# Kernel tuning notes

Measured on AMD Instinct MI355X. Metric: run time of the kernel, lower is better.

Reference implementation:

```python
import jax, jax.numpy as jnp
import numpy as np

EPS = 1e-5
NH = 8          # num_heads
WT_LEVELS = 5


def ln(x, w, b):
    m = jnp.mean(x, -1, keepdims=True)
    v = jnp.mean((x - m) ** 2, -1, keepdims=True)
    return (x - m) / jnp.sqrt(v + EPS) * w + b


def gelu(x):
    return jax.nn.gelu(x, approximate=False)  # torch nn.GELU default (erf)


def dwconv(x, w, b, stride, padding):
    # x: [B,C,H,W], w: [kh,kw,1,C] depthwise
    C = x.shape[1]
    y = jax.lax.conv_general_dilated(x, w, (stride, stride), padding,
                                     dimension_numbers=('NCHW', 'HWIO', 'NCHW'),
                                     feature_group_count=C)
    return y if b is None else y + b[None, :, None, None]


def conv2d(x, w, b, padding='SAME'):
    y = jax.lax.conv_general_dilated(x, w, (1, 1), padding,
                                     dimension_numbers=('NCHW', 'HWIO', 'NCHW'))
    return y + b[None, :, None, None]


def haar_dwt(x):
    # orthonormal 2x2 Haar analysis via even/odd slicing (no conv needed)
    a = x[..., 0::2, 0::2]; b = x[..., 0::2, 1::2]
    c = x[..., 1::2, 0::2]; d = x[..., 1::2, 1::2]
    ll = (a + b + c + d) * 0.5
    lh = (-a - b + c + d) * 0.5
    hl = (-a + b - c + d) * 0.5
    hh = (a - b - c + d) * 0.5
    return ll, lh, hl, hh


def haar_idwt(ll, lh, hl, hh):
    a = (ll - lh - hl + hh) * 0.5
    b = (ll - lh + hl - hh) * 0.5
    c = (ll + lh - hl - hh) * 0.5
    d = (ll + lh + hl + hh) * 0.5
    B, C, H, W = ll.shape
    top = jnp.stack([a, b], -1).reshape(B, C, H, 2 * W)
    bot = jnp.stack([c, d], -1).reshape(B, C, H, 2 * W)
    return jnp.stack([top, bot], -2).reshape(B, C, 2 * H, 2 * W)


def wtconv(x, base_w, base_b, base_scale, wav_w, wav_scale):
    # WTConv2d (Haar, wt_levels=5, kernel 3, depthwise): multi-level wavelet
    # decomposition, depthwise 3x3 conv + scale at each level, reconstruction,
    # added to a scaled depthwise base conv.
    B, C = x.shape[0], x.shape[1]
    lls, hs, shapes = [], [], []
    cur = x
    for i in range(WT_LEVELS):
        shapes.append(cur.shape)
        Hc, Wc = cur.shape[2], cur.shape[3]
        if Hc % 2 or Wc % 2:
            cur = jnp.pad(cur, ((0, 0), (0, 0), (0, Hc % 2), (0, Wc % 2)))
        sub = jnp.stack(haar_dwt(cur), 2)                # [B,C,4,h,w]
        cur = sub[:, :, 0]
        h, w = sub.shape[3], sub.shape[4]
        t = sub.reshape(B, C * 4, h, w)
        t = dwconv(t, wav_w[i], None, 1, 'SAME') * wav_scale[i][None, :, None, None]
        t = t.reshape(B, C, 4, h, w)
        lls.append(t[:, :, 0])
        hs.append(t[:, :, 1:4])
    nxt = 0.0
    for i in range(WT_LEVELS - 1, -1, -1):
        ll = lls[i] + nxt
        h3 = hs[i]
        nxt = haar_idwt(ll, h3[:, :, 0], h3[:, :, 1], h3[:, :, 2])
        sh = shapes[i]
        nxt = nxt[:, :, :sh[2], :sh[3]]
    base = dwconv(x, base_w, base_b, 1, 'SAME') * base_scale[None, :, None, None]
    return base + nxt


def block_forward(x, H, W, ln1_w, ln1_b, ln2_w, ln2_b, q_w, kv1_w, kv2_w,
                  sr1_w, sr1_b, sr2_w, sr2_b, an1_w, an1_b, an2_w, an2_b,
                  wt_base_w, wt_base_b, wt_base_scale, wt_wav_w, wt_wav_scale,
                  cp2d_w, cp2d_b, cn_w, cn_b, proj_w, proj_b,
                  fc1_w, fc1_b, fc2_w, fc2_b):
    B, N, C0 = x.shape
    Cp = C0 // 4            # conv/wavelet part channels
    Ca = C0 - Cp            # attention part channels (3/4)
    hd = Ca // NH
    scale = hd ** -0.5

    xin = ln(x, ln1_w, ln1_b)
    xc, xa = xin[..., :Cp], xin[..., Cp:]

    # --- wavelet-conv branch ---
    xc = xc.reshape(B, H, W, Cp).transpose(0, 3, 1, 2)        # [B,Cp,H,W]
    xc = wtconv(xc, wt_base_w, wt_base_b, wt_base_scale, wt_wav_w, wt_wav_scale)
    xc = conv2d(xc, cp2d_w, cp2d_b, 'SAME')                   # k3 p1 (sr_ratio=8)
    xc = gelu(ln(xc.reshape(B, Cp, N).transpose(0, 2, 1), cn_w, cn_b))  # [B,N,Cp]

    # --- multi-scale spatial-reduction attention (sr_ratio=8) ---
    q = (xa @ q_w).reshape(B, N, NH, hd).transpose(0, 2, 1, 3)  # [B,NH,N,hd]
    x_ = xa.transpose(0, 2, 1).reshape(B, Ca, H, W)
    x1 = gelu(ln(dwconv(x_, sr1_w, sr1_b, 8, 'VALID').reshape(B, Ca, -1)
                 .transpose(0, 2, 1), an1_w, an1_b))           # [B,49,Ca]
    x2 = gelu(ln(dwconv(x_, sr2_w, sr2_b, 4, 'VALID').reshape(B, Ca, -1)
                 .transpose(0, 2, 1), an2_w, an2_b))           # [B,196,Ca]

    def branch(xs, kv_w, qh):
        L = xs.shape[1]
        kv = (xs @ kv_w).reshape(B, L, 2, NH // 2, hd).transpose(2, 0, 3, 1, 4)
        k, v = kv[0], kv[1]
        a = jax.nn.softmax(jnp.einsum('bhnd,bhld->bhnl', qh, k) * scale, axis=-1)
        return jnp.einsum('bhnl,bhld->bhnd', a, v).transpose(0, 2, 1, 3).reshape(B, N, Ca // 2)

    y1 = branch(x1, kv1_w, q[:, :NH // 2])
    y2 = branch(x2, kv2_w, q[:, NH // 2:])

    attn_out = jnp.concatenate([y1, y2, xc], -1) @ proj_w + proj_b

    x = x + attn_out
    m = ln(x, ln2_w, ln2_b)
    return x + (gelu(m @ fc1_w + fc1_b) @ fc2_w + fc2_b)


def setup_inputs() -> dict:
    key = jax.random.key(0)
    ks = jax.random.split(key, 16)
    B, H, W, C0 = 32, 56, 56, 128
    N = H * W
    Cp, Ca = C0 // 4, C0 // 4 * 3

    def nrm(k, shape, std=0.02):
        return jax.random.normal(k, shape, jnp.float32) * std

    return dict(
        x=jax.random.normal(ks[0], (B, N, C0), jnp.float32),
        H=H, W=W,
        ln1_w=jnp.ones((C0,)), ln1_b=jnp.zeros((C0,)),
        ln2_w=jnp.ones((C0,)), ln2_b=jnp.zeros((C0,)),
        q_w=nrm(ks[1], (Ca, Ca)),
        kv1_w=nrm(ks[2], (Ca, Ca)),
        kv2_w=nrm(ks[3], (Ca, Ca)),
        sr1_w=nrm(ks[4], (8, 8, 1, Ca), 0.05), sr1_b=jnp.zeros((Ca,)),
        sr2_w=nrm(ks[5], (4, 4, 1, Ca), 0.05), sr2_b=jnp.zeros((Ca,)),
        an1_w=jnp.ones((Ca,)), an1_b=jnp.zeros((Ca,)),
        an2_w=jnp.ones((Ca,)), an2_b=jnp.zeros((Ca,)),
        wt_base_w=nrm(ks[6], (3, 3, 1, Cp), 0.1), wt_base_b=jnp.zeros((Cp,)),
        wt_base_scale=jnp.ones((Cp,)),
        wt_wav_w=nrm(ks[7], (5, 3, 3, 1, 4 * Cp), 0.1),
        wt_wav_scale=jnp.full((5, 4 * Cp), 0.1, jnp.float32),
        cp2d_w=nrm(ks[8], (3, 3, Cp, Cp), 0.05), cp2d_b=jnp.zeros((Cp,)),
        cn_w=jnp.ones((Cp,)), cn_b=jnp.zeros((Cp,)),
        proj_w=nrm(ks[9], (C0, C0)), proj_b=jnp.zeros((C0,)),
        fc1_w=nrm(ks[10], (C0, 4 * C0)), fc1_b=jnp.zeros((4 * C0,)),
        fc2_w=nrm(ks[11], (4 * C0, C0)), fc2_b=jnp.zeros((C0,)),
    )


def reference(x, H, W, ln1_w, ln1_b, ln2_w, ln2_b, q_w, kv1_w, kv2_w,
              sr1_w, sr1_b, sr2_w, sr2_b, an1_w, an1_b, an2_w, an2_b,
              wt_base_w, wt_base_b, wt_base_scale, wt_wav_w, wt_wav_scale,
              cp2d_w, cp2d_b, cn_w, cn_b, proj_w, proj_b,
              fc1_w, fc1_b, fc2_w, fc2_b):
    return block_forward(x, H, W, ln1_w, ln1_b, ln2_w, ln2_b, q_w, kv1_w, kv2_w,
                         sr1_w, sr1_b, sr2_w, sr2_b, an1_w, an1_b, an2_w, an2_b,
                         wt_base_w, wt_base_b, wt_base_scale, wt_wav_w, wt_wav_scale,
                         cp2d_w, cp2d_b, cn_w, cn_b, proj_w, proj_b,
                         fc1_w, fc1_b, fc2_w, fc2_b)
```

## Files before the change

kernel.cpp:

```cpp
#include <hip/hip_runtime.h>
#include <hip/hip_bf16.h>
#include <math.h>

typedef __hip_bfloat16 bf16;
typedef __attribute__((ext_vector_type(8))) short bf16x8;
typedef __attribute__((ext_vector_type(4))) float f32x4;

#define Bc   32
#define Hc   56
#define Wcc  56
#define Nc   3136
#define Cpc  32
#define Cac  96
#define EPSc 1e-5f
#define SCALEc 0.28867513459481287f

__device__ __forceinline__ float gelu_f(float x) {
    return 0.5f * x * (1.0f + erff(x * 0.7071067811865475f));
}

__device__ __forceinline__ float fast_exp2(float x) {
#if defined(__has_builtin)
#if __has_builtin(__builtin_amdgcn_exp2f)
    return __builtin_amdgcn_exp2f(x);
#else
    return exp2f(x);
#endif
#else
    return exp2f(x);
#endif
}

__global__ __launch_bounds__(256) void ln1_kernel(const float* __restrict__ x,
        const float* __restrict__ g, const float* __restrict__ be,
        float* __restrict__ xa, bf16* __restrict__ xab, float* __restrict__ xc_img)
{
    int wv = threadIdx.x >> 6, lane = threadIdx.x & 63;
    int row = blockIdx.x * 4 + wv;
    if (row >= Bc * Nc) return;
    const float* xr = x + (size_t)row * 128;
    float x0 = xr[lane];
    float x1 = xr[lane + 64];
    float s = x0 + x1, q = x0 * x0 + x1 * x1;
    for (int o = 32; o; o >>= 1) { s += __shfl_xor(s, o); q += __shfl_xor(q, o); }
    float mean = s * (1.f / 128.f);
    float inv = rsqrtf(q * (1.f / 128.f) - mean * mean + EPSc);
    int b = row / Nc, n = row % Nc;
    {
        int c = lane;
        float y = (x0 - mean) * inv * g[c] + be[c];
        if (c < Cpc) xc_img[(size_t)(b * Cpc + c) * Nc + n] = y;
        else { xa[(size_t)row * Cac + (c - Cpc)] = y;
               xab[(size_t)row * Cac + (c - Cpc)] = __float2bfloat16(y); }
    }
    {
        int c = lane + 64;
        float y = (x1 - mean) * inv * g[c] + be[c];
        xa[(size_t)row * Cac + (c - Cpc)] = y;
        xab[(size_t)row * Cac + (c - Cpc)] = __float2bfloat16(y);
    }
}

__global__ void dwt_kernel(const float* __restrict__ src, int cs, int h, int w,
                           int h2, int w2, float* __restrict__ sub)
{
    int t = blockIdx.x * blockDim.x + threadIdx.x;
    int total = Bc * 32 * h2 * w2;
    if (t >= total) return;
    int xx = t % w2; int r = t / w2;
    int yy = r % h2; r /= h2;
    int c = r & 31; int b = r >> 5;
    const float* sp = src + (size_t)cs * (b * 32 + c) * h * w;
    int y0 = yy * 2, x0 = xx * 2;
    bool xe = (x0 + 1 < w), ye = (y0 + 1 < h);
    float a  = sp[y0 * w + x0];
    float bb = xe ? sp[y0 * w + x0 + 1] : 0.f;
    float cc = ye ? sp[(y0 + 1) * w + x0] : 0.f;
    float dd = (xe && ye) ? sp[(y0 + 1) * w + x0 + 1] : 0.f;
    size_t pl = (size_t)h2 * w2;
    size_t ob = (size_t)(b * 128 + c * 4) * pl + yy * w2 + xx;
    sub[ob]          = ( a + bb + cc + dd) * 0.5f;
    sub[ob + pl]     = (-a - bb + cc + dd) * 0.5f;
    sub[ob + 2 * pl] = (-a + bb - cc + dd) * 0.5f;
    sub[ob + 3 * pl] = ( a - bb - cc + dd) * 0.5f;
}

template<int H>
__device__ __forceinline__ void dw3_body(int r, const float* __restrict__ src,
        const float* __restrict__ wt, const float* __restrict__ scale,
        float* __restrict__ dst)
{
    int x = r % H; int rr = r / H;
    int y = rr % H; rr /= H;
    int c = rr & 127;
    const float* sp = src + (r - x - y * H);
    float acc = 0.f;
    #pragma unroll
    for (int u = 0; u < 3; u++) {
        int yy = y + u - 1;
        if (yy < 0 || yy >= H) continue;
        #pragma unroll
        for (int v = 0; v < 3; v++) {
            int xx = x + v - 1;
            if (xx < 0 || xx >= H) continue;
            acc += sp[yy * H + xx] * wt[(u * 3 + v) * 128 + c];
        }
    }
    dst[r] = acc * scale[c];
}

__global__ void dw3x3_all_kernel(const float* __restrict__ sub, const float* __restrict__ wavw,
        const float* __restrict__ wavs, float* __restrict__ tt)
{
    int t = blockIdx.x * blockDim.x + threadIdx.x;
    if (t < 3211264)      dw3_body<28>(t,           sub,           wavw,        wavs,       tt);
    else if (t < 4014080) dw3_body<14>(t - 3211264, sub + 3211264, wavw + 1152, wavs + 128, tt + 3211264);
    else if (t < 4214784) dw3_body<7> (t - 4014080, sub + 4014080, wavw + 2304, wavs + 256, tt + 4014080);
    else if (t < 4280320) dw3_body<4> (t - 4214784, sub + 4214784, wavw + 3456, wavs + 384, tt + 4214784);
    else if (t < 4296704) dw3_body<2> (t - 4280320, sub + 4280320, wavw + 4608, wavs + 512, tt + 4280320);
}

__global__ void idwt_kernel(const float* __restrict__ tl, const float* __restrict__ nxt,
        float* __restrict__ outp, int h2, int w2, int ho, int wo)
{
    int t = blockIdx.x * blockDim.x + threadIdx.x;
    int total = Bc * 32 * ho * wo;
    if (t >= total) return;
    int x = t % wo; int r = t / wo;
    int y = r % ho; r /= ho;
    int c = r & 31; int b = r >> 5;
    int y2 = y >> 1, x2 = x >> 1;
    size_t pl = (size_t)h2 * w2;
    size_t base = (size_t)(b * 128 + c * 4) * pl + y2 * w2 + x2;
    float ll = tl[base];
    if (nxt) ll += nxt[(size_t)(b * 32 + c) * pl + y2 * w2 + x2];
    float lh = tl[base + pl], hl = tl[base + 2 * pl], hh = tl[base + 3 * pl];
    float v;
    if ((y & 1) == 0) v = ((x & 1) == 0) ? (ll - lh - hl + hh) : (ll - lh + hl - hh);
    else              v = ((x & 1) == 0) ? (ll + lh - hl - hh) : (ll + lh + hl + hh);
    outp[t] = v * 0.5f;
}

__global__ void idwt_dwbase_kernel(const float* __restrict__ tl, const float* __restrict__ nxt,
        const float* __restrict__ src, const float* __restrict__ wt,
        const float* __restrict__ scale, const float* __restrict__ bias,
        bf16* __restrict__ dst_nhwc)
{
    int t = blockIdx.x * blockDim.x + threadIdx.x;
    if (t >= Bc * 32 * Nc) return;
    int x = t % Wcc; int r = t / Wcc;
    int y = r % Hc; r /= Hc;
    int c = r & 31; int b = r >> 5;
    int y2 = y >> 1, x2 = x >> 1;
    const size_t pl = 784;
    size_t base = (size_t)(b * 128 + c * 4) * pl + y2 * 28 + x2;
    float ll = tl[base] + nxt[(size_t)(b * 32 + c) * pl + y2 * 28 + x2];
    float lh = tl[base + pl], hl = tl[base + 2 * pl], hh = tl[base + 3 * pl];
    float v;
    if ((y & 1) == 0) v = ((x & 1) == 0) ? (ll - lh - hl + hh) : (ll - lh + hl - hh);
    else              v = ((x & 1) == 0) ? (ll + lh - hl - hh) : (ll + lh + hl + hh);
    float recon = v * 0.5f;
    const float* sp = src + (t - x - y * Wcc);
    float acc = 0.f;
    #pragma unroll
    for (int u = 0; u < 3; u++) {
        int yy = y + u - 1;
        if (yy < 0 || yy >= Hc) continue;
        #pragma unroll
        for (int vv2 = 0; vv2 < 3; vv2++) {
            int xx = x + vv2 - 1;
            if (xx < 0 || xx >= Wcc) continue;
            acc += sp[yy * Wcc + xx] * wt[(u * 3 + vv2) * 32 + c];
        }
    }
    acc = (acc + bias[c]) * scale[c] + recon;
    dst_nhwc[(((size_t)b * Hc + y) * Wcc + x) * 32 + c] = __float2bfloat16(acc);
}

__global__ void wprep_kernel(const float* __restrict__ qw, const float* __restrict__ kv1w,
        const float* __restrict__ kv2w, const float* __restrict__ pw,
        const float* __restrict__ f1w, const float* __restrict__ f2w,
        const float* __restrict__ cpw, bf16* __restrict__ qwt, bf16* __restrict__ kv1wt,
        bf16* __restrict__ kv2wt, bf16* __restrict__ pwt, bf16* __restrict__ w1t,
        bf16* __restrict__ w2t, bf16* __restrict__ cpwt)
{
    int t = blockIdx.x * blockDim.x + threadIdx.x;
    if (t < 9216) {
        int n = t % 96, k = t / 96;
        qwt[n * 96 + k] = __float2bfloat16(qw[t]);
    } else if (t < 18432) {
        int u = t - 9216; int n = u % 96, k = u / 96;
        kv1wt[n * 96 + k] = __float2bfloat16(kv1w[u]);
    } else if (t < 27648) {
        int u = t - 18432; int n = u % 96, k = u / 96;
        kv2wt[n * 96 + k] = __float2bfloat16(kv2w[u]);
    } else if (t < 44032) {
        int u = t - 27648; int n = u % 128, k = u / 128;
        pwt[n * 128 + k] = __float2bfloat16(pw[u]);
    } else if (t < 109568) {
        int u = t - 44032; int n = u % 512, k = u / 512;
        w1t[(size_t)n * 128 + k] = __float2bfloat16(f1w[u]);
    } else if (t < 175104) {
        int u = t - 109568; int n = u % 128, k = u / 128;
        w2t[(size_t)n * 512 + k] = __float2bfloat16(f2w[u]);
    } else if (t < 184320) {
        int u = t - 175104; int co = u / 288, k = u % 288;
        cpwt[u] = __float2bfloat16(cpw[k * 32 + co]);
    }
}

__global__ __launch_bounds__(256) void cp2d_cn_kernel(const bf16* __restrict__ src,
        const bf16* __restrict__ wtc, const float* __restrict__ bias,
        const float* __restrict__ cnw, const float* __restrict__ cnb,
        bf16* __restrict__ attn_cat)
{
    __shared__ unsigned short in_s[10 * 400];
    __shared__ unsigned short w_s[32 * 296];
    int tid = threadIdx.x;
    int b = blockIdx.y;
    int ty = blockIdx.x / 7, tx = blockIdx.x % 7;
    for (int idx = tid; idx < 1152; idx += 256) {
        int co = idx / 36, j8 = (idx % 36) * 8;
        *(int4*)&w_s[co * 296 + j8] = *(const int4*)(wtc + co * 288 + j8);
    }
    {
        int idx = tid;
        if (idx < 200) {
            int cell = idx >> 1, half = idx & 1;
            int dy = cell / 10, dx = cell % 10;
            int gy = ty * 8 - 1 + dy, gx = tx * 8 - 1 + dx;
            int4 v0 = make_int4(0, 0, 0, 0), v1 = v0;
            if (gy >= 0 && gy < 56 && gx >= 0 && gx < 56) {
                const int4* gp = (const int4*)(src + ((((size_t)b * 56 + gy) * 56 + gx) * 32 + half * 16));
                v0 = gp[0]; v1 = gp[1];
            }
            *(int4*)&in_s[dy * 400 + dx * 40 + half * 16] = v0;
            *(int4*)&in_s[dy * 400 + dx * 40 + half * 16 + 8] = v1;
        }
    }
    __syncthreads();
    int wave = tid >> 6, lane = tid & 63;
    int ml = lane & 15, qd = lane >> 4;
    int m = wave * 16 + ml;
    int ly = m >> 3, lx = m & 7;
    f32x4 acc0 = {0.f, 0.f, 0.f, 0.f}, acc1 = {0.f, 0.f, 0.f, 0.f};
    #pragma unroll
    for (int u = 0; u < 3; u++)
    #pragma unroll
    for (int v = 0; v < 3; v++) {
        bf16x8 af = *(const bf16x8*)&in_s[(ly + u) * 400 + (lx + v) * 40 + qd * 8];
        int k = (u * 3 + v) * 32 + qd * 8;
        bf16x8 b0 = *(const bf16x8*)&w_s[ml * 296 + k];
        bf16x8 b1 = *(const bf16x8*)&w_s[(16 + ml) * 296 + k];
        acc0 = __builtin_amdgcn_mfma_f32_16x16x32_bf16(af, b0, acc0, 0, 0, 0);
        acc1 = __builtin_amdgcn_mfma_f32_16x16x32_bf16(af, b1, acc1, 0, 0, 0);
    }
    float bia0 = bias[ml], bia1 = bias[16 + ml];
    float g0 = cnw[ml], g1 = cnw[16 + ml];
    float be0 = cnb[ml], be1 = cnb[16 + ml];
    #pragma unroll
    for (int r = 0; r < 4; r++) {
        float c0 = acc0[r] + bia0;
        float c1 = acc1[r] + bia1;
        float s = c0 + c1, q = c0 * c0 + c1 * c1;
        #pragma unroll
        for (int o = 8; o; o >>= 1) { s += __shfl_xor(s, o); q += __shfl_xor(q, o); }
        float mean = s * (1.f / 32.f);
        float inv = rsqrtf(q * (1.f / 32.f) - mean * mean + EPSc);
        int mr = wave * 16 + qd * 4 + r;
        int ry = ty * 8 + (mr >> 3), rx = tx * 8 + (mr & 7);
        bf16* op = attn_cat + ((size_t)b * Nc + ry * 56 + rx) * 128 + 96;
        op[ml]      = __float2bfloat16(gelu_f((c0 - mean) * inv * g0 + be0));
        op[16 + ml] = __float2bfloat16(gelu_f((c1 - mean) * inv * g1 + be1));
    }
}

template<int KS, int LD>
__device__ __forceinline__ void sr_body(int t, const float* __restrict__ xa,
        const float* __restrict__ wt, const float* __restrict__ bias,
        float* __restrict__ outp)
{
    int c = t % Cac; int r = t / Cac;
    int j = r % LD; r /= LD;
    int i = r % LD; int b = r / LD;
    float acc = bias[c];
    for (int u = 0; u < KS; u++)
        for (int v = 0; v < KS; v++)
            acc += xa[(size_t)(b * Nc + (i * KS + u) * Wcc + (j * KS + v)) * Cac + c]
                 * wt[(u * KS + v) * Cac + c];
    outp[t] = acc;
}

__global__ void sr_all_kernel(const float* __restrict__ xa,
        const float* __restrict__ sr1w, const float* __restrict__ sr1b, float* __restrict__ x1p,
        const float* __restrict__ sr2w, const float* __restrict__ sr2b, float* __restrict__ x2p)
{
    int t = blockIdx.x * blockDim.x + threadIdx.x;
    if (t < 150528) sr_body<8, 7>(t, xa, sr1w, sr1b, x1p);
    else {
        int u = t - 150528;
        if (u < 602112) sr_body<4, 14>(u, xa, sr2w, sr2b, x2p);
    }
}

__global__ __launch_bounds__(256) void ln96_all_kernel(
        const float* __restrict__ s1, const float* __restrict__ g1,
        const float* __restrict__ b1, bf16* __restrict__ d1,
        const float* __restrict__ s2, const float* __restrict__ g2,
        const float* __restrict__ b2, bf16* __restrict__ d2)
{
    int wv = threadIdx.x >> 6, lane = threadIdx.x & 63;
    int row = blockIdx.x * 4 + wv;
    const float* sp; const float* g; const float* be; bf16* dst; int r;
    if (row < 1568)      { sp = s1; g = g1; be = b1; dst = d1; r = row; }
    else if (row < 7840) { sp = s2; g = g2; be = b2; dst = d2; r = row - 1568; }
    else return;
    sp += (size_t)r * 96;
    float x0 = sp[lane];
    float x1 = (lane < 32) ? sp[64 + lane] : 0.f;
    float s = x0 + x1, q = x0 * x0 + x1 * x1;
    for (int o = 32; o; o >>= 1) { s += __shfl_xor(s, o); q += __shfl_xor(q, o); }
    float mean = s * (1.f / 96.f);
    float inv = rsqrtf(q * (1.f / 96.f) - mean * mean + EPSc);
    dst[(size_t)r * 96 + lane] =
        __float2bfloat16(gelu_f((x0 - mean) * inv * g[lane] + be[lane]));
    if (lane < 32)
        dst[(size_t)r * 96 + 64 + lane] =
            __float2bfloat16(gelu_f((x1 - mean) * inv * g[64 + lane] + be[64 + lane]));
}

__global__ __launch_bounds__(256) void ln2_kernel(const float* __restrict__ xres,
        const float* __restrict__ g, const float* __restrict__ be,
        bf16* __restrict__ xnb)
{
    int wv = threadIdx.x >> 6, lane = threadIdx.x & 63;
    int row = blockIdx.x * 4 + wv;
    if (row >= Bc * Nc) return;
    const float* xr = xres + (size_t)row * 128;
    float x0 = xr[lane], x1 = xr[lane + 64];
    float s = x0 + x1, q = x0 * x0 + x1 * x1;
    for (int o = 32; o; o >>= 1) { s += __shfl_xor(s, o); q += __shfl_xor(q, o); }
    float mean = s * (1.f / 128.f);
    float inv = rsqrtf(q * (1.f / 128.f) - mean * mean + EPSc);
    xnb[(size_t)row * 128 + lane] =
        __float2bfloat16((x0 - mean) * inv * g[lane] + be[lane]);
    xnb[(size_t)row * 128 + lane + 64] =
        __float2bfloat16((x1 - mean) * inv * g[lane + 64] + be[lane + 64]);
}

template<int NF, bool GELU, bool RES, int OMODE>
__global__ __launch_bounds__(256) void gemm_kernel(const bf16* __restrict__ A,
        const bf16* __restrict__ Wt, const float* __restrict__ bias,
        const float* __restrict__ res, void* __restrict__ outp,
        int M, int K, int Nt)
{
    constexpr int TN = 16 * NF;
    __shared__ unsigned short As[64][40];
    __shared__ unsigned short Bs[TN][40];
    int tid = threadIdx.x;
    int wave = tid >> 6, lane = tid & 63;
    int m0 = blockIdx.y * 64, n0 = blockIdx.x * TN;
    f32x4 acc[NF];
    #pragma unroll
    for (int f = 0; f < NF; f++) acc[f] = (f32x4){0.f, 0.f, 0.f, 0.f};

    int ar = tid >> 2, ac = (tid & 3) << 3;
    int ml = wave * 16 + (lane & 15);
    int qd = lane >> 4;

    for (int k0 = 0; k0 < K; k0 += 32) {
        int4 av = make_int4(0, 0, 0, 0);
        if (m0 + ar < M) av = *(const int4*)(A + (size_t)(m0 + ar) * K + k0 + ac);
        *(int4*)&As[ar][ac] = av;
        for (int idx = tid; idx < TN * 4; idx += 256) {
            int br = idx >> 2, bc = (idx & 3) << 3;
            *(int4*)&Bs[br][bc] = *(const int4*)(Wt + (size_t)(n0 + br) * K + k0 + bc);
        }
        __syncthreads();
        bf16x8 af = *(const bf16x8*)&As[ml][qd * 8];
        #pragma unroll
        for (int f = 0; f < NF; f++) {
            bf16x8 bfv = *(const bf16x8*)&Bs[f * 16 + (lane & 15)][qd * 8];
            acc[f] = __builtin_amdgcn_mfma_f32_16x16x32_bf16(af, bfv, acc[f], 0, 0, 0);
        }
        __syncthreads();
    }
    #pragma unroll
    for (int f = 0; f < NF; f++) {
        int n = n0 + f * 16 + (lane & 15);
        #pragma unroll
        for (int r = 0; r < 4; r++) {
            int m = m0 + wave * 16 + qd * 4 + r;
            if (m >= M) continue;
            float v = acc[f][r];
            if (bias) v += bias[n];
            if (GELU) v = gelu_f(v);
            if (RES)  v += res[(size_t)m * Nt + n];
            if (OMODE == 1)
                ((bf16*)outp)[(size_t)m * Nt + n] = __float2bfloat16(v);
            else if (OMODE == 2) {
                int b = m / Nc, nn = m - b * Nc;
                int h = n / 12, d = n - h * 12;
                ((float*)outp)[(((size_t)(b * 8 + h)) * Nc + nn) * 12 + d] = v;
            } else
                ((float*)outp)[(size_t)m * Nt + n] = v;
        }
    }
}

template<int L>
__device__ __forceinline__ void attn_body(const float* __restrict__ qh,
        const float* __restrict__ kv, int hl, int h, int b,
        float* kb, float* vb, bf16* __restrict__ attn_cat)
{
    for (int idx = threadIdx.x; idx < L * 3; idx += 256) {
        int l = idx / 3, f = idx % 3;
        const float4* kp = (const float4*)(kv + (size_t)(b * L + l) * 96 + hl * 12) + f;
        float4 kk = kp[0];
        float4 vv = kp[12];
        *(float4*)&kb[l * 12 + f * 4] = kk;
        *(float4*)&vb[l * 12 + f * 4] = vv;
    }
    int n = blockIdx.x * 256 + threadIdx.x;
    bool act = (n < Nc);
    int nn = act ? n : (Nc - 1);
    const float4* qp = (const float4*)(qh + (((size_t)(b * 8 + h)) * Nc + nn) * 12);
    float4 q0 = qp[0], q1 = qp[1], q2 = qp[2];
    const float PRE = SCALEc * 1.4426950408889634f;
    q0.x *= PRE; q0.y *= PRE; q0.z *= PRE; q0.w *= PRE;
    q1.x *= PRE; q1.y *= PRE; q1.z *= PRE; q1.w *= PRE;
    q2.x *= PRE; q2.y *= PRE; q2.z *= PRE; q2.w *= PRE;
    __syncthreads();

    float den = 0.f;
    float o[12];
    #pragma unroll
    for (int d = 0; d < 12; d++) o[d] = 0.f;

    #pragma unroll 4
    for (int l = 0; l < L; l++) {
        const float4 k0 = *(const float4*)&kb[l * 12];
        const float4 k1 = *(const float4*)&kb[l * 12 + 4];
        const float4 k2 = *(const float4*)&kb[l * 12 + 8];
        float s0 = q0.x * k0.x + q0.y * k0.y + q0.z * k0.z + q0.w * k0.w;
        float s1 = q1.x * k1.x + q1.y * k1.y + q1.z * k1.z + q1.w * k1.w;
        float s2 = q2.x * k2.x + q2.y * k2.y + q2.z * k2.z + q2.w * k2.w;
        float e = fast_exp2(s0 + s1 + s2);
        den += e;
        const float4 v0 = *(const float4*)&vb[l * 12];
        const float4 v1 = *(const float4*)&vb[l * 12 + 4];
        const float4 v2 = *(const float4*)&vb[l * 12 + 8];
        o[0] += e * v0.x; o[1]  += e * v0.y; o[2]  += e * v0.z; o[3]  += e * v0.w;
        o[4] += e * v1.x; o[5]  += e * v1.y; o[6]  += e * v1.z; o[7]  += e * v1.w;
        o[8] += e * v2.x; o[9]  += e * v2.y; o[10] += e * v2.z; o[11] += e * v2.w;
    }
    if (act) {
        float rden = 1.f / den;
        bf16* op = attn_cat + (size_t)(b * Nc + n) * 128 + h * 12;
        #pragma unroll
        for (int d = 0; d < 12; d++) op[d] = __float2bfloat16(o[d] * rden);
    }
}

__global__ __launch_bounds__(256) void attn_kernel(const float* __restrict__ qh,
        const float* __restrict__ kv1, const float* __restrict__ kv2,
        bf16* __restrict__ attn_cat)
{
    __shared__ float kb[196 * 12];
    __shared__ float vb[196 * 12];
    int h = blockIdx.y, b = blockIdx.z;
    if (h < 4) attn_body<49> (qh, kv1, h,     h, b, kb, vb, attn_cat);
    else       attn_body<196>(qh, kv2, h - 4, h, b, kb, vb, attn_cat);
}

extern "C" void kernel_launch(void* const* d_in, const int* in_sizes, int n_in,
                              void* d_out, int out_size, void* d_ws, size_t ws_size,
                              hipStream_t stream)
{
    const float* x    = (const float*)d_in[0];
    const float* ln1w = (const float*)d_in[3];
    const float* ln1b = (const float*)d_in[4];
    const float* ln2w = (const float*)d_in[5];
    const float* ln2b = (const float*)d_in[6];
    const float* qw   = (const float*)d_in[7];
    const float* kv1w = (const float*)d_in[8];
    const float* kv2w = (const float*)d_in[9];
    const float* sr1w = (const float*)d_in[10];
    const float* sr1b = (const float*)d_in[11];
    const float* sr2w = (const float*)d_in[12];
    const float* sr2b = (const float*)d_in[13];
    const float* an1w = (const float*)d_in[14];
    const float* an1b = (const float*)d_in[15];
    const float* an2w = (const float*)d_in[16];
    const float* an2b = (const float*)d_in[17];
    const float* wbw  = (const float*)d_in[18];
    const float* wbb  = (const float*)d_in[19];
    const float* wbs  = (const float*)d_in[20];
    const float* wavw = (const float*)d_in[21];
    const float* wavs = (const float*)d_in[22];
    const float* cpw  = (const float*)d_in[23];
    const float* cpb  = (const float*)d_in[24];
    const float* cnw  = (const float*)d_in[25];
    const float* cnb  = (const float*)d_in[26];
    const float* pw   = (const float*)d_in[27];
    const float* pb   = (const float*)d_in[28];
    const float* f1w  = (const float*)d_in[29];
    const float* f1b  = (const float*)d_in[30];
    const float* f2w  = (const float*)d_in[31];
    const float* f2b  = (const float*)d_in[32];
    float* dout = (float*)d_out;
    float* ws = (float*)d_ws;

    float* XA    = ws;
    float* QB    = ws + 9633792;
    float* XRES  = ws;
    bf16*  XNb   = (bf16*)(ws + 12845056);
    bf16*  XAb   = (bf16*)(ws + 19267584);
    bf16*  ACATb = (bf16*)(ws + 24084480);
    float* XCI   = ws + 30507008;
    float* SUB   = ws + 33718272;
    float* TT    = ws + 38014976;
    float* RA    = ws + 42311680;
    float* RB    = ws + 45522944;
    float* X1P   = ws + 48734208;
    float* X2P   = ws + 48884736;
    bf16*  X1Bb  = (bf16*)(ws + 49486848);
    bf16*  X2Bb  = (bf16*)(ws + 49562112);
    float* KV1   = ws + 49863168;
    float* KV2   = ws + 50013696;
    bf16*  WTB   = (bf16*)(ws + 50615808);
    bf16*  qwt   = WTB;
    bf16*  kv1wt = WTB + 9216;
    bf16*  kv2wt = WTB + 18432;
    bf16*  pwt   = WTB + 27648;
    bf16*  w1t   = WTB + 44032;
    bf16*  w2t   = WTB + 109568;
    bf16*  cpwt  = WTB + 175104;
    bf16*  Hb    = (bf16*)(ws + 24084480);
    bf16*  CIMGb = (bf16*)SUB;
    float* S0 = SUB;            float* T0 = TT;
    float* S1 = SUB + 3211264;  float* T1 = TT + 3211264;
    float* S2 = SUB + 4014080;  float* T2 = TT + 4014080;
    float* S3 = SUB + 4214784;  float* T3 = TT + 4214784;
    float* S4 = SUB + 4280320;  float* T4 = TT + 4280320;

    wprep_kernel<<<720, 256, 0, stream>>>(qw, kv1w, kv2w, pw, f1w, f2w, cpw,
                                          qwt, kv1wt, kv2wt, pwt, w1t, w2t, cpwt);

    ln1_kernel<<<25088, 256, 0, stream>>>(x, ln1w, ln1b, XA, XAb, XCI);

    dwt_kernel<<<3136, 256, 0, stream>>>(XCI, 1, 56, 56, 28, 28, S0);
    dwt_kernel<<<784,  256, 0, stream>>>(S0, 4, 28, 28, 14, 14, S1);
    dwt_kernel<<<196,  256, 0, stream>>>(S1, 4, 14, 14, 7, 7,   S2);
    dwt_kernel<<<64,   256, 0, stream>>>(S2, 4, 7, 7,   4, 4,   S3);
    dwt_kernel<<<16,   256, 0, stream>>>(S3, 4, 4, 4,   2, 2,   S4);

    dw3x3_all_kernel<<<16784, 256, 0, stream>>>(SUB, wavw, wavs, TT);

    idwt_kernel<<<64,   256, 0, stream>>>(T4, nullptr, RA, 2, 2, 4, 4);
    idwt_kernel<<<196,  256, 0, stream>>>(T3, RA, RB, 4, 4, 7, 7);
    idwt_kernel<<<784,  256, 0, stream>>>(T2, RB, RA, 7, 7, 14, 14);
    idwt_kernel<<<3136, 256, 0, stream>>>(T1, RA, RB, 14, 14, 28, 28);

    idwt_dwbase_kernel<<<12544, 256, 0, stream>>>(T0, RB, XCI, wbw, wbs, wbb, CIMGb);

    cp2d_cn_kernel<<<dim3(49, 32), 256, 0, stream>>>(CIMGb, cpwt, cpb, cnw, cnb, ACATb);

    sr_all_kernel<<<2940, 256, 0, stream>>>(XA, sr1w, sr1b, X1P, sr2w, sr2b, X2P);

    ln96_all_kernel<<<1960, 256, 0, stream>>>(X1P, an1w, an1b, X1Bb,
                                              X2P, an2w, an2b, X2Bb);

    gemm_kernel<6,false,false,2><<<dim3(1, 1568), 256, 0, stream>>>(XAb,  qwt,   nullptr, nullptr, QB,  100352, 96, 96);
    gemm_kernel<6,false,false,0><<<dim3(1, 25),   256, 0, stream>>>(X1Bb, kv1wt, nullptr, nullptr, KV1, 1568,   96, 96);
    gemm_kernel<6,false,false,0><<<dim3(1, 98),   256, 0, stream>>>(X2Bb, kv2wt, nullptr, nullptr, KV2, 6272,   96, 96);

    attn_kernel<<<dim3(13, 8, 32), 256, 0, stream>>>(QB, KV1, KV2, ACATb);

    gemm_kernel<4,false,true,0><<<dim3(2, 1568), 256, 0, stream>>>(ACATb, pwt, pb, x, XRES, 100352, 128, 128);

    ln2_kernel<<<25088, 256, 0, stream>>>(XRES, ln2w, ln2b, XNb);

    gemm_kernel<4,true,false,1><<<dim3(8, 1568), 256, 0, stream>>>(XNb, w1t, f1b, nullptr, Hb, 100352, 128, 512);

    gemm_kernel<4,false,true,0><<<dim3(2, 1568), 256, 0, stream>>>(Hb, w2t, f2b, XRES, dout, 100352, 512, 128);
}
```

Measured before the change: 630.4 us.

## Fuse projection GEMM with residual add and LayerNorm, widen GEMM K-tile

Replaces the separate projection GEMM and ln2 kernel with one kernel that computes a full 128-wide output row tile per block, adds bias and residual, then does the LayerNorm in registers via cross-lane shuffles before writing both the fp32 residual and the bf16 normalized output. This drops one launch and a full read of the fp32 residual tensor. Separately, the generic GEMM gains a K-tile template parameter, and the MLP GEMMs use 64-wide K tiles to halve the number of barrier/load iterations. The cost is more shared memory per block, which may lower occupancy.

```diff
diff --git a/kernel.cpp b/kernel.cpp
--- a/kernel.cpp
+++ b/kernel.cpp
@@ -329,34 +329,15 @@
             __float2bfloat16(gelu_f((x1 - mean) * inv * g[64 + lane] + be[64 + lane]));
 }
 
-__global__ __launch_bounds__(256) void ln2_kernel(const float* __restrict__ xres,
-        const float* __restrict__ g, const float* __restrict__ be,
-        bf16* __restrict__ xnb)
-{
-    int wv = threadIdx.x >> 6, lane = threadIdx.x & 63;
-    int row = blockIdx.x * 4 + wv;
-    if (row >= Bc * Nc) return;
-    const float* xr = xres + (size_t)row * 128;
-    float x0 = xr[lane], x1 = xr[lane + 64];
-    float s = x0 + x1, q = x0 * x0 + x1 * x1;
-    for (int o = 32; o; o >>= 1) { s += __shfl_xor(s, o); q += __shfl_xor(q, o); }
-    float mean = s * (1.f / 128.f);
-    float inv = rsqrtf(q * (1.f / 128.f) - mean * mean + EPSc);
-    xnb[(size_t)row * 128 + lane] =
-        __float2bfloat16((x0 - mean) * inv * g[lane] + be[lane]);
-    xnb[(size_t)row * 128 + lane + 64] =
-        __float2bfloat16((x1 - mean) * inv * g[lane + 64] + be[lane + 64]);
-}
-
-template<int NF, bool GELU, bool RES, int OMODE>
+template<int NF, int BK, bool GELU, bool RES, int OMODE>
 __global__ __launch_bounds__(256) void gemm_kernel(const bf16* __restrict__ A,
         const bf16* __restrict__ Wt, const float* __restrict__ bias,
         const float* __restrict__ res, void* __restrict__ outp,
         int M, int K, int Nt)
 {
     constexpr int TN = 16 * NF;
-    __shared__ unsigned short As[64][40];
-    __shared__ unsigned short Bs[TN][40];
+    __shared__ unsigned short As[64][BK + 8];
+    __shared__ unsigned short Bs[TN][BK + 8];
     int tid = threadIdx.x;
     int wave = tid >> 6, lane = tid & 63;
     int m0 = blockIdx.y * 64, n0 = blockIdx.x * TN;
@@ -368,20 +349,27 @@
     int ml = wave * 16 + (lane & 15);
     int qd = lane >> 4;
 
-    for (int k0 = 0; k0 < K; k0 += 32) {
-        int4 av = make_int4(0, 0, 0, 0);
-        if (m0 + ar < M) av = *(const int4*)(A + (size_t)(m0 + ar) * K + k0 + ac);
-        *(int4*)&As[ar][ac] = av;
-        for (int idx = tid; idx < TN * 4; idx += 256) {
-            int br = idx >> 2, bc = (idx & 3) << 3;
+    for (int k0 = 0; k0 < K; k0 += BK) {
+        #pragma unroll
+        for (int i = 0; i < BK / 32; i++) {
+            int cc = ac + i * 32;
+            int4 av = make_int4(0, 0, 0, 0);
+            if (m0 + ar < M) av = *(const int4*)(A + (size_t)(m0 + ar) * K + k0 + cc);
+            *(int4*)&As[ar][cc] = av;
+        }
+        for (int idx = tid; idx < TN * (BK / 8); idx += 256) {
+            int br = idx / (BK / 8), bc = (idx % (BK / 8)) * 8;
             *(int4*)&Bs[br][bc] = *(const int4*)(Wt + (size_t)(n0 + br) * K + k0 + bc);
         }
         __syncthreads();
-        bf16x8 af = *(const bf16x8*)&As[ml][qd * 8];
-        #pragma unroll
-        for (int f = 0; f < NF; f++) {
-            bf16x8 bfv = *(const bf16x8*)&Bs[f * 16 + (lane & 15)][qd * 8];
-            acc[f] = __builtin_amdgcn_mfma_f32_16x16x32_bf16(af, bfv, acc[f], 0, 0, 0);
+        #pragma unroll
+        for (int kk = 0; kk < BK / 32; kk++) {
+            bf16x8 af = *(const bf16x8*)&As[ml][kk * 32 + qd * 8];
+            #pragma unroll
+            for (int f = 0; f < NF; f++) {
+                bf16x8 bfv = *(const bf16x8*)&Bs[f * 16 + (lane & 15)][kk * 32 + qd * 8];
+                acc[f] = __builtin_amdgcn_mfma_f32_16x16x32_bf16(af, bfv, acc[f], 0, 0, 0);
+            }
         }
         __syncthreads();
     }
@@ -404,6 +392,77 @@
                 ((float*)outp)[(((size_t)(b * 8 + h)) * Nc + nn) * 12 + d] = v;
             } else
                 ((float*)outp)[(size_t)m * Nt + n] = v;
+        }
+    }
+}
+
+__global__ __launch_bounds__(256) void proj_ln_kernel(const bf16* __restrict__ A,
+        const bf16* __restrict__ Wt, const float* __restrict__ bias,
+        const float* __restrict__ res, const float* __restrict__ g,
+        const float* __restrict__ be, float* __restrict__ xres, bf16* __restrict__ xnb)
+{
+    __shared__ unsigned short As[64][72];
+    __shared__ unsigned short Bs[128][72];
+    int tid = threadIdx.x;
+    int wave = tid >> 6, lane = tid & 63;
+    int m0 = blockIdx.x * 64;
+    f32x4 acc[8];
+    #pragma unroll
+    for (int f = 0; f < 8; f++) acc[f] = (f32x4){0.f, 0.f, 0.f, 0.f};
+
+    int ar = tid >> 2, ac = (tid & 3) << 3;
+    int ml = lane & 15, qd = lane >> 4;
+    int mlw = wave * 16 + ml;
+
+    for (int k0 = 0; k0 < 128; k0 += 64) {
+        #pragma unroll
+        for (int i = 0; i < 2; i++) {
+            int cc = ac + i * 32;
+            *(int4*)&As[ar][cc] = *(const int4*)(A + (size_t)(m0 + ar) * 128 + k0 + cc);
+        }
+        for (int idx = tid; idx < 1024; idx += 256) {
+            int br = idx >> 3, bc = (idx & 7) * 8;
+            *(int4*)&Bs[br][bc] = *(const int4*)(Wt + (size_t)br * 128 + k0 + bc);
+        }
+        __syncthreads();
+        #pragma unroll
+        for (int kk = 0; kk < 2; kk++) {
+            bf16x8 af = *(const bf16x8*)&As[mlw][kk * 32 + qd * 8];
+            #pragma unroll
+            for (int f = 0; f < 8; f++) {
+                bf16x8 bfv = *(const bf16x8*)&Bs[f * 16 + ml][kk * 32 + qd * 8];
+                acc[f] = __builtin_amdgcn_mfma_f32_16x16x32_bf16(af, bfv, acc[f], 0, 0, 0);
+            }
+        }
+        __syncthreads();
+    }
+    float bia[8], gg[8], bb[8];
+    #pragma unroll
+    for (int f = 0; f < 8; f++) {
+        int n = f * 16 + ml;
+        bia[f] = bias[n]; gg[f] = g[n]; bb[f] = be[n];
+    }
+    #pragma unroll
+    for (int r = 0; r < 4; r++) {
+        int m = m0 + wave * 16 + qd * 4 + r;
+        float vv[8];
+        float s = 0.f, q = 0.f;
+        #pragma unroll
+        for (int f = 0; f < 8; f++) {
+            int n = f * 16 + ml;
+            float v = acc[f][r] + bia[f] + res[(size_t)m * 128 + n];
+            vv[f] = v; s += v; q += v * v;
+        }
+        #pragma unroll
+        for (int o = 8; o; o >>= 1) { s += __shfl_xor(s, o); q += __shfl_xor(q, o); }
+        float mean = s * (1.f / 128.f);
+        float inv = rsqrtf(q * (1.f / 128.f) - mean * mean + EPSc);
+        #pragma unroll
+        for (int f = 0; f < 8; f++) {
+            int n = f * 16 + ml;
+            xres[(size_t)m * 128 + n] = vv[f];
+            xnb[(size_t)m * 128 + n] =
+                __float2bfloat16((vv[f] - mean) * inv * gg[f] + bb[f]);
         }
     }
 }
@@ -571,17 +630,15 @@
     ln96_all_kernel<<<1960, 256, 0, stream>>>(X1P, an1w, an1b, X1Bb,
                                               X2P, an2w, an2b, X2Bb);
 
-    gemm_kernel<6,false,false,2><<<dim3(1, 1568), 256, 0, stream>>>(XAb,  qwt,   nullptr, nullptr, QB,  100352, 96, 96);
-    gemm_kernel<6,false,false,0><<<dim3(1, 25),   256, 0, stream>>>(X1Bb, kv1wt, nullptr, nullptr, KV1, 1568,   96, 96);
-    gemm_kernel<6,false,false,0><<<dim3(1, 98),   256, 0, stream>>>(X2Bb, kv2wt, nullptr, nullptr, KV2, 6272,   96, 96);
+    gemm_kernel<6,32,false,false,2><<<dim3(1, 1568), 256, 0, stream>>>(XAb,  qwt,   nullptr, nullptr, QB,  100352, 96, 96);
+    gemm_kernel<6,32,false,false,0><<<dim3(1, 25),   256, 0, stream>>>(X1Bb, kv1wt, nullptr, nullptr, KV1, 1568,   96, 96);
+    gemm_kernel<6,32,false,false,0><<<dim3(1, 98),   256, 0, stream>>>(X2Bb, kv2wt, nullptr, nullptr, KV2, 6272,   96, 96);
 
     attn_kernel<<<dim3(13, 8, 32), 256, 0, stream>>>(QB, KV1, KV2, ACATb);
 
-    gemm_kernel<4,false,true,0><<<dim3(2, 1568), 256, 0, stream>>>(ACATb, pwt, pb, x, XRES, 100352, 128, 128);
-
-    ln2_kernel<<<25088, 256, 0, stream>>>(XRES, ln2w, ln2b, XNb);
-
-    gemm_kernel<4,true,false,1><<<dim3(8, 1568), 256, 0, stream>>>(XNb, w1t, f1b, nullptr, Hb, 100352, 128, 512);
-
-    gemm_kernel<4,false,true,0><<<dim3(2, 1568), 256, 0, stream>>>(Hb, w2t, f2b, XRES, dout, 100352, 512, 128);
-}
+    proj_ln_kernel<<<1568, 256, 0, stream>>>(ACATb, pwt, pb, x, ln2w, ln2b, XRES, XNb);
+
+    gemm_kernel<4,64,true,false,1><<<dim3(8, 1568), 256, 0, stream>>>(XNb, w1t, f1b, nullptr, Hb, 100352, 128, 512);
+
+    gemm_kernel<4,64,false,true,0><<<dim3(2, 1568), 256, 0, stream>>>(Hb, w2t, f2b, XRES, dout, 100352, 512, 128);
+}
```

Result: faster. 607.3 us (-3.7%).
